# Kernel optimization log

Measured on AMD Instinct MI355X. Metric: run time of the kernel, lower is better.

Reference implementation:

```python
import jax, jax.numpy as jnp
import numpy as np

B, V, T = 1024, 50000, 50  # batch, n_items, max tail length

def setup_inputs() -> dict:
    key = jax.random.key(0)
    k1, k2, k3, k4 = jax.random.split(key, 4)
    output = jax.random.normal(k1, (B, V), dtype=jnp.float32)
    target = jax.random.randint(k2, (B,), 0, V, dtype=jnp.int32)
    tails = jax.random.randint(k3, (B, T), 0, V, dtype=jnp.int32)
    tail_len = jax.random.randint(k4, (B,), 0, T, dtype=jnp.int32)  # some rows have 0 -> empty tail
    return {"output": output, "target": target, "tails": tails, "tail_len": tail_len}


def reference(output, target, tails, tail_len):
    # output: [B, V] float scores; target: [B] int; tails: [B, T] padded indices; tail_len: [B]
    target_scores = jnp.take_along_axis(output, target[:, None].astype(jnp.int32), axis=1)[:, 0]  # [B]
    exp_out = jnp.exp(output)
    total_exp = jnp.sum(exp_out, axis=1)  # [B]  (torch: sum(exp(output), 1))
    log_pl = target_scores - jnp.log(total_exp)  # [B]

    # --- ragged tail term, vectorized over rows ---
    s = jnp.take_along_axis(output, tails, axis=1)          # [B, T] tail scores
    mask = jnp.arange(T)[None, :] < tail_len[:, None]       # [B, T] valid positions
    es = jnp.where(mask, jnp.exp(s), 0.0)                   # exp of valid tail scores
    above = jnp.sum(jnp.where(mask, s, 0.0), axis=1)        # [B] sum of tail scores
    # remaining mass: total - exp(target) - sum(exp(tail scores))
    others = total_exp - jnp.exp(target_scores) - jnp.sum(es, axis=1)  # [B]

    # torch flips the valid tail then cumsums exp; with padding at the end,
    # flipping the full padded row puts (zero-contribution) pads first, so the
    # cumsum at valid positions matches the valid-only reversed cumsum.
    fe = es[:, ::-1]                                        # [B, T]
    fmask = mask[:, ::-1]
    c = jnp.cumsum(fe, axis=1)                              # [B, T]
    lg = jnp.log(c + others[:, None])
    below_sum = jnp.sum(jnp.where(fmask, lg, 0.0), axis=1)  # [B]
    tail_term = jnp.where(tail_len > 0, above - below_sum, 0.0)  # rows with empty tail skipped

    neg_like = -(log_pl + tail_term)                        # [B]
    return neg_like
```

## Files before the change

### kernel.cpp

```cpp
#include <hip/hip_runtime.h>

#define BB 1024
#define VV 50000
#define TT 50
#define NTH 1024
#define N4  12500
#define FULL_ITERS 12
#define REM (N4 - FULL_ITERS * NTH)

__global__ __launch_bounds__(NTH) void listmle_fused_kernel(
    const float* __restrict__ output,
    const int*   __restrict__ target,
    const int*   __restrict__ tails,
    const int*   __restrict__ tail_len,
    float*       __restrict__ out)
{
    const int r   = blockIdx.x;
    const int tid = threadIdx.x;
    const float* __restrict__ row = output + (size_t)r * VV;
    const float4* __restrict__ p = (const float4*)row;

    float4 v[FULL_ITERS];
    #pragma unroll
    for (int u = 0; u < FULL_ITERS; ++u) v[u] = p[tid + NTH * u];
    const bool has_rem = tid < REM;
    float4 vt = make_float4(0.f, 0.f, 0.f, 0.f);
    if (has_rem) vt = p[tid + NTH * FULL_ITERS];

    float s0 = 0.f, s1 = 0.f, s2 = 0.f, s3 = 0.f;
    #pragma unroll
    for (int u = 0; u < FULL_ITERS; ++u) {
        s0 += __expf(v[u].x);
        s1 += __expf(v[u].y);
        s2 += __expf(v[u].z);
        s3 += __expf(v[u].w);
    }
    if (has_rem) {
        s0 += __expf(vt.x);
        s1 += __expf(vt.y);
        s2 += __expf(vt.z);
        s3 += __expf(vt.w);
    }
    float sum = (s0 + s1) + (s2 + s3);

    #pragma unroll
    for (int off = 32; off > 0; off >>= 1)
        sum += __shfl_down(sum, off, 64);

    __shared__ float wsum[16];
    __shared__ float s_s[TT];
    __shared__ float es_s[TT];
    __shared__ float total_s;

    const int lane = tid & 63;
    const int wave = tid >> 6;
    if (lane == 0) wsum[wave] = sum;

    const int L = tail_len[r];
    if (tid >= 64 && tid < 64 + TT) {
        const int j = tid - 64;
        float sv = 0.f, ev = 0.f;
        if (j < L) {
            sv = row[tails[r * TT + j]];
            ev = __expf(sv);
        }
        s_s[j]  = sv;
        es_s[j] = ev;
    }
    __syncthreads();

    if (tid == 0) {
        float t = 0.f;
        #pragma unroll
        for (int w = 0; w < 16; ++w) t += wsum[w];
        total_s = t;
    }
    __syncthreads();

    if (tid == 0) {
        const float total = total_s;
        const float ts = row[target[r]];
        const float log_pl = ts - __logf(total);

        float above = 0.f, sum_es = 0.f;
        for (int j = 0; j < L; ++j) {
            above  += s_s[j];
            sum_es += es_s[j];
        }
        const float others = total - __expf(ts) - sum_es;

        float run = 0.f, below = 0.f;
        for (int k = L - 1; k >= 0; --k) {
            run += es_s[k];
            below += __logf(run + others);
        }
        const float tail_term = (L > 0) ? (above - below) : 0.f;
        out[r] = -(log_pl + tail_term);
    }
}

extern "C" void kernel_launch(void* const* d_in, const int* in_sizes, int n_in,
                              void* d_out, int out_size, void* d_ws, size_t ws_size,
                              hipStream_t stream) {
    const float* output   = (const float*)d_in[0];
    const int*   target   = (const int*)d_in[1];
    const int*   tails    = (const int*)d_in[2];
    const int*   tail_len = (const int*)d_in[3];
    float*       out      = (float*)d_out;

    listmle_fused_kernel<<<BB, NTH, 0, stream>>>(output, target, tails, tail_len, out);
}
```

Baseline: 281.6 us.

## Split row exp-sum into segmented blocks and a separate wave-per-row tail kernel

Splits the fused per-row kernel into two launches. The first uses four 256-thread blocks per row to compute partial exp-sums into workspace. The second assigns one wavefront per row, which combines the partials and computes the tail term with shuffle reductions and a wave-level suffix scan instead of a serial single-thread loop. This removes the serialized tail computation and block-wide barriers that sat on the critical path, at the cost of an extra launch and a workspace round trip.

```diff
diff --git a/kernel.cpp b/kernel.cpp
--- a/kernel.cpp
+++ b/kernel.cpp
@@ -3,33 +3,35 @@
 #define BB 1024
 #define VV 50000
 #define TT 50
-#define NTH 1024
-#define N4  12500
-#define FULL_ITERS 12
-#define REM (N4 - FULL_ITERS * NTH)
 
-__global__ __launch_bounds__(NTH) void listmle_fused_kernel(
+#define SEGS    4
+#define SEG4    3125
+#define P1_NTH  256
+#define P1_FULL 12
+#define P1_REM  (SEG4 - P1_FULL * P1_NTH)
+
+__global__ __launch_bounds__(P1_NTH) void rowsum_exp_kernel(
     const float* __restrict__ output,
-    const int*   __restrict__ target,
-    const int*   __restrict__ tails,
-    const int*   __restrict__ tail_len,
-    float*       __restrict__ out)
+    float*       __restrict__ partials)
 {
-    const int r   = blockIdx.x;
+    const int bid = blockIdx.x;
+    const int r   = bid >> 2;
+    const int seg = bid & 3;
     const int tid = threadIdx.x;
-    const float* __restrict__ row = output + (size_t)r * VV;
-    const float4* __restrict__ p = (const float4*)row;
 
-    float4 v[FULL_ITERS];
+    const float4* __restrict__ p =
+        (const float4*)(output + (size_t)r * VV) + seg * SEG4;
+
+    float4 v[P1_FULL];
     #pragma unroll
-    for (int u = 0; u < FULL_ITERS; ++u) v[u] = p[tid + NTH * u];
-    const bool has_rem = tid < REM;
+    for (int u = 0; u < P1_FULL; ++u) v[u] = p[tid + P1_NTH * u];
+    const bool has_rem = tid < P1_REM;
     float4 vt = make_float4(0.f, 0.f, 0.f, 0.f);
-    if (has_rem) vt = p[tid + NTH * FULL_ITERS];
+    if (has_rem) vt = p[tid + P1_NTH * P1_FULL];
 
     float s0 = 0.f, s1 = 0.f, s2 = 0.f, s3 = 0.f;
     #pragma unroll
-    for (int u = 0; u < FULL_ITERS; ++u) {
+    for (int u = 0; u < P1_FULL; ++u) {
         s0 += __expf(v[u].x);
         s1 += __expf(v[u].y);
         s2 += __expf(v[u].z);
@@ -47,54 +49,68 @@
     for (int off = 32; off > 0; off >>= 1)
         sum += __shfl_down(sum, off, 64);
 
-    __shared__ float wsum[16];
-    __shared__ float s_s[TT];
-    __shared__ float es_s[TT];
-    __shared__ float total_s;
-
+    __shared__ float wsum[4];
     const int lane = tid & 63;
     const int wave = tid >> 6;
     if (lane == 0) wsum[wave] = sum;
+    __syncthreads();
+    if (tid == 0)
+        partials[bid] = (wsum[0] + wsum[1]) + (wsum[2] + wsum[3]);
+}
 
+#define P2_NTH 256
+
+__global__ __launch_bounds__(P2_NTH) void tail_kernel(
+    const float* __restrict__ output,
+    const int*   __restrict__ target,
+    const int*   __restrict__ tails,
+    const int*   __restrict__ tail_len,
+    const float* __restrict__ partials,
+    float*       __restrict__ out)
+{
+    const int wave = threadIdx.x >> 6;
+    const int lane = threadIdx.x & 63;
+    const int r    = blockIdx.x * 4 + wave;
+
+    const float* __restrict__ row = output + (size_t)r * VV;
     const int L = tail_len[r];
-    if (tid >= 64 && tid < 64 + TT) {
-        const int j = tid - 64;
-        float sv = 0.f, ev = 0.f;
-        if (j < L) {
-            sv = row[tails[r * TT + j]];
-            ev = __expf(sv);
-        }
-        s_s[j]  = sv;
-        es_s[j] = ev;
+
+    float tot = (lane < SEGS) ? partials[r * SEGS + lane] : 0.f;
+    #pragma unroll
+    for (int off = 32; off > 0; off >>= 1)
+        tot += __shfl_xor(tot, off, 64);
+
+    const float ts     = row[target[r]];
+    const float log_pl = ts - __logf(tot);
+
+    float sv = 0.f, ev = 0.f;
+    if (lane < L) {
+        sv = row[tails[r * TT + lane]];
+        ev = __expf(sv);
     }
-    __syncthreads();
 
-    if (tid == 0) {
-        float t = 0.f;
-        #pragma unroll
-        for (int w = 0; w < 16; ++w) t += wsum[w];
-        total_s = t;
+    float a = sv, e = ev;
+    #pragma unroll
+    for (int off = 32; off > 0; off >>= 1) {
+        a += __shfl_xor(a, off, 64);
+        e += __shfl_xor(e, off, 64);
     }
-    __syncthreads();
+    const float others = tot - __expf(ts) - e;
 
-    if (tid == 0) {
-        const float total = total_s;
-        const float ts = row[target[r]];
-        const float log_pl = ts - __logf(total);
+    float run = ev;
+    #pragma unroll
+    for (int off = 1; off < 64; off <<= 1) {
+        float o = __shfl_down(run, off, 64);
+        if (lane + off < 64) run += o;
+    }
 
-        float above = 0.f, sum_es = 0.f;
-        for (int j = 0; j < L; ++j) {
-            above  += s_s[j];
-            sum_es += es_s[j];
-        }
-        const float others = total - __expf(ts) - sum_es;
+    float bl = (lane < L) ? __logf(run + others) : 0.f;
+    #pragma unroll
+    for (int off = 32; off > 0; off >>= 1)
+        bl += __shfl_xor(bl, off, 64);
 
-        float run = 0.f, below = 0.f;
-        for (int k = L - 1; k >= 0; --k) {
-            run += es_s[k];
-            below += __logf(run + others);
-        }
-        const float tail_term = (L > 0) ? (above - below) : 0.f;
+    if (lane == 0) {
+        const float tail_term = (L > 0) ? (a - bl) : 0.f;
         out[r] = -(log_pl + tail_term);
     }
 }
@@ -107,6 +123,9 @@
     const int*   tails    = (const int*)d_in[2];
     const int*   tail_len = (const int*)d_in[3];
     float*       out      = (float*)d_out;
+    float*       partials = (float*)d_ws;
 
-    listmle_fused_kernel<<<BB, NTH, 0, stream>>>(output, target, tails, tail_len, out);
+    rowsum_exp_kernel<<<BB * SEGS, P1_NTH, 0, stream>>>(output, partials);
+    tail_kernel<<<BB / 4, P2_NTH, 0, stream>>>(output, target, tails, tail_len,
+                                               partials, out);
 }
```

Result: no change. 280.9 us (-0.2%).
